# Performance work log

Measured on AMD Instinct MI355X. Metric: run time of the kernel, lower is better.

Reference implementation:

```python
import jax, jax.numpy as jnp
from jax import lax
import numpy as np

# correlation hyperparams (from init_kwargs)
MAX_D = 32      # maxDisplacement
PAD = 1         # zero padding
K = 3           # patch (kernel) size
STRIDE_K = 1    # stride over output pixels
STRIDE_D = 1    # stride over displacements


def setup_inputs() -> dict:
    key = jax.random.key(0)
    k0, k1 = jax.random.split(key)
    x0 = jax.random.normal(k0, (4, 64, 256, 512), dtype=jnp.float32)
    x1 = jax.random.normal(k1, (4, 64, 256, 512), dtype=jnp.float32)
    return {"x0": x0, "x1": x1}


def _corr2d(x0, x1):
    # x0, x1: [B, C, H, W] NCHW feature maps
    B, C, H, W = x0.shape
    # zero-pad spatially; x1 gets extra width padding so all displacements are in-bounds
    x0p = jnp.pad(x0, ((0, 0), (0, 0), (PAD, PAD), (PAD, PAD)))
    x1p = jnp.pad(x1, ((0, 0), (0, 0), (PAD, PAD), (PAD + MAX_D, PAD + MAX_D)))
    Wp = W + 2 * PAD
    # width offsets into x1p for displacements d = -MAX_D .. MAX_D step STRIDE_D
    offsets = jnp.arange(0, 2 * MAX_D + 1, STRIDE_D, dtype=jnp.int32)

    def step(carry, off):
        x1s = lax.dynamic_slice_in_dim(x1p, off, Wp, axis=3)   # [B,C,Hp,Wp]
        prod = jnp.sum(x0p * x1s, axis=1)                      # channel dot -> [B,Hp,Wp]
        # KxK box-sum over the patch, stride STRIDE_K -> [B,Ho,Wo]
        s = lax.reduce_window(prod, jnp.float32(0), lax.add,
                              (1, K, K), (1, STRIDE_K, STRIDE_K), 'VALID')
        return carry, s

    _, out = lax.scan(step, None, offsets)        # [nD, B, Ho, Wo]
    out = jnp.transpose(out, (1, 0, 2, 3))        # [B, nD, Ho, Wo]
    return out / jnp.asarray(K * K * C, out.dtype)


def reference(x0, x1):
    return _corr2d(x0, x1)
```

## Files before the change

kernel.cpp:

```cpp
#include <hip/hip_runtime.h>

#define WF 512
#define HF 256
#define CF 64
#define NDTOT 65
#define DP 72
#define APAD 40

static constexpr size_t CH  = (size_t)HF * WF;
static constexpr size_t WH  = (size_t)HF * WF;
static constexpr float  INV = 1.0f / 576.0f;

typedef _Float16 f16;
typedef _Float16 f16x2 __attribute__((ext_vector_type(2)));
typedef _Float16 f16x4 __attribute__((ext_vector_type(4)));
typedef _Float16 f16x8 __attribute__((ext_vector_type(8)));
typedef float    f32x4 __attribute__((ext_vector_type(4)));

__global__ __launch_bounds__(256, 2)
void corr_gram(const float* __restrict__ x0, const float* __restrict__ x1,
               f16* __restrict__ ws) {
    const int f = blockIdx.x;
    const int xcd = f & 7;
    const int strip = (f >> 3) & 3;
    const int pl = f >> 5;
    const int pair = xcd * 128 + pl;
    const int y = pair & 255;
    const int b = pair >> 8;

    const int t = threadIdx.x;
    const int l = t & 63;
    const int w = t >> 6;
    const int X0 = strip << 7;
    const int jb = X0 - 32;

    const int n  = l & 15;
    const int kq = l >> 4;

    __shared__ f16 S[12800];
    f16* SA = S;
    f16* SB = S + 5120;

    const float* x0r = x0 + (size_t)b * CF * CH + (size_t)y * WF;
    const float* x1r = x1 + (size_t)b * CF * CH + (size_t)y * WF;

    const int c4  = t & 31;
    const int chq = t >> 5;
    int bchp[3], bc4b[3], bcol[3]; bool bok[3];
#pragma unroll
    for (int u = 0; u < 3; ++u) {
        const int idx = u * 256 + t;
        bchp[u] = idx / 48;
        bc4b[u] = idx - 48 * bchp[u];
        bcol[u] = jb + 4 * bc4b[u];
        bok[u]  = (unsigned)bcol[u] < (unsigned)WF;
    }

#define LOADH(h, A4, B4) do { \
    const float* xa = x0r + (size_t)((h) * 32 + 4 * chq) * CH + (X0 + 4 * c4); \
    _Pragma("unroll") \
    for (int j = 0; j < 4; ++j) A4[j] = *(const f32x4*)(xa + (size_t)j * CH); \
    _Pragma("unroll") \
    for (int u = 0; u < 3; ++u) { \
        const float* xb = x1r + (size_t)((h) * 32 + 2 * bchp[u]) * CH + bcol[u]; \
        B4[2*u]     = bok[u] ? *(const f32x4*)xb        : (f32x4)0.f; \
        B4[2*u + 1] = bok[u] ? *(const f32x4*)(xb + CH) : (f32x4)0.f; \
    } \
} while (0)

#define CVTW(A4, B4) do { \
    _Pragma("unroll") \
    for (int j2 = 0; j2 < 4; ++j2) { \
        f16x4 v; \
        v[0] = (f16)A4[0][j2]; v[1] = (f16)A4[1][j2]; \
        v[2] = (f16)A4[2][j2]; v[3] = (f16)A4[3][j2]; \
        *(f16x4*)&SA[(4 * c4 + j2) * APAD + 4 * chq] = v; \
    } \
    _Pragma("unroll") \
    for (int u = 0; u < 3; ++u) { \
        _Pragma("unroll") \
        for (int j2 = 0; j2 < 4; ++j2) { \
            f16x2 v; \
            v[0] = (f16)B4[2*u][j2]; v[1] = (f16)B4[2*u + 1][j2]; \
            *(f16x2*)&SB[(4 * bc4b[u] + j2) * APAD + 2 * bchp[u]] = v; \
        } \
    } \
} while (0)

#define COMP() do { \
    const f16x8 a0 = *(const f16x8*)&SA[(w * 32 + n) * APAD + kq * 8]; \
    const f16x8 a1 = *(const f16x8*)&SA[(w * 32 + 16 + n) * APAD + kq * 8]; \
    _Pragma("unroll") \
    for (int jt = 0; jt < 6; ++jt) { \
        const f16x8 bf = *(const f16x8*)&SB[(w * 32 + jt * 16 + n) * APAD + kq * 8]; \
        if (jt < 5) \
            acc[jt] = __builtin_amdgcn_mfma_f32_16x16x32_f16(a0, bf, acc[jt], 0, 0, 0); \
        if (jt >= 1) \
            acc[4 + jt] = __builtin_amdgcn_mfma_f32_16x16x32_f16(a1, bf, acc[4 + jt], 0, 0, 0); \
    } \
} while (0)

    f32x4 acc[10];
#pragma unroll
    for (int i = 0; i < 10; ++i) acc[i] = (f32x4)0.0f;

    f32x4 a4[4], b4[6], a4n[4], b4n[6];

    LOADH(0, a4, b4);
    CVTW(a4, b4);
    __syncthreads();
    LOADH(1, a4n, b4n);
    COMP();
    __syncthreads();
    CVTW(a4n, b4n);
    __syncthreads();
    COMP();
    __syncthreads();

#undef COMP
#undef CVTW
#undef LOADH

    f16* eb = S + w * 2304;
#pragma unroll
    for (int xt = 0; xt < 2; ++xt) {
#pragma unroll
        for (int p = 0; p < 5; ++p) {
            const int i = xt * 5 + p;
#pragma unroll
            for (int q = 0; q < 4; ++q) {
                const int m = kq * 4 + q;
                const int xl = xt * 16 + m;
                const int d = 16 * p + n - m;
                if ((unsigned)d < (unsigned)NDTOT)
                    eb[xl * DP + d] = (f16)acc[i][q];
            }
        }
    }
#pragma unroll
    for (int i = 0; i < 4; ++i) {
        const int idx = l + 64 * i;
        if (idx < 224) {
            const int xl = idx / 7;
            eb[xl * DP + NDTOT + (idx - 7 * xl)] = (f16)0.f;
        }
    }
    uint4* dst = (uint4*)(ws + ((size_t)(b * HF + y) * WF + X0 + w * 32) * DP);
    const uint4* src = (const uint4*)eb;
#pragma unroll
    for (int i = 0; i < 5; ++i) {
        const int idx = l + 64 * i;
        if (idx < 288) dst[idx] = src[idx];
    }
}

__global__ __launch_bounds__(256)
void corr_box(const f16* __restrict__ ws, float* __restrict__ out) {
    const int xt = blockIdx.x;
    const int yt = blockIdx.y;
    const int b = blockIdx.z;
    const int t = threadIdx.x;
    const int x0b = xt * 32, y0 = yt * 8;

    __shared__ f16 S[10 * 34][DP];

    for (int u = 0; u < 10; ++u) {
        const int yy = y0 - 1 + u;
        const bool yok = (unsigned)yy < (unsigned)HF;
        const f16* src = ws + ((size_t)(b * HF + yy) * WF + (x0b - 1)) * DP;
#pragma unroll
        for (int sub = 0; sub < 2; ++sub) {
            const int idx = sub * 256 + t;
            if (idx < 306) {
                const int v = idx / 9, dg = idx - v * 9;
                const int xx = x0b - 1 + v;
                f16x8 val;
#pragma unroll
                for (int jj = 0; jj < 8; ++jj) val[jj] = (f16)0.f;
                if (yok && (unsigned)xx < (unsigned)WF)
                    val = *(const f16x8*)(src + (size_t)v * DP + dg * 8);
                *(f16x8*)&S[u * 34 + v][dg * 8] = val;
            }
        }
    }
    __syncthreads();

    const int ly = t >> 5, lx = t & 31;
    const int yg = y0 + ly, xg = x0b + lx;
    float* o0 = out + (size_t)b * NDTOT * WH + (size_t)yg * WF + xg;

#pragma unroll 1
    for (int dg = 0; dg < 9; ++dg) {
        f16x8 s;
#pragma unroll
        for (int jj = 0; jj < 8; ++jj) s[jj] = (f16)0.f;
#pragma unroll
        for (int du = 0; du < 3; ++du)
#pragma unroll
            for (int dv = 0; dv < 3; ++dv)
                s += *(const f16x8*)&S[(ly + du) * 34 + (lx + dv)][dg * 8];
#pragma unroll
        for (int jj = 0; jj < 8; ++jj) {
            const int d = dg * 8 + jj;
            if (d < NDTOT) o0[(size_t)d * WH] = (float)s[jj] * INV;
        }
    }
}

__global__ void corr_naive(const float* __restrict__ x0, const float* __restrict__ x1,
                           float* __restrict__ out) {
    const size_t total = (size_t)4 * NDTOT * WH;
    size_t idx = (size_t)blockIdx.x * blockDim.x + threadIdx.x;
    if (idx >= total) return;
    const int j = (int)(idx % WF);
    const int i = (int)((idx / WF) % HF);
    const int d = (int)((idx / WH) % NDTOT);
    const int b = (int)(idx / ((size_t)NDTOT * WH));
    const int disp = d - 32;
    float s = 0.f;
    for (int u = i - 1; u <= i + 1; ++u) {
        if (u < 0 || u >= HF) continue;
        for (int v = j - 1; v <= j + 1; ++v) {
            if (v < 0 || v >= WF) continue;
            const int v1c = v + disp;
            if (v1c < 0 || v1c >= WF) continue;
            const float* p0 = x0 + (size_t)b * CF * CH + (size_t)u * WF + v;
            const float* p1 = x1 + (size_t)b * CF * CH + (size_t)u * WF + v1c;
            for (int c = 0; c < CF; ++c)
                s += p0[(size_t)c * CH] * p1[(size_t)c * CH];
        }
    }
    out[idx] = s * INV;
}

extern "C" void kernel_launch(void* const* d_in, const int* in_sizes, int n_in,
                              void* d_out, int out_size, void* d_ws, size_t ws_size,
                              hipStream_t stream) {
    const float* x0 = (const float*)d_in[0];
    const float* x1 = (const float*)d_in[1];
    float* out = (float*)d_out;

    const size_t wsNeed = (size_t)4 * HF * WF * DP * sizeof(f16);

    if (ws_size >= wsNeed) {
        f16* ws = (f16*)d_ws;
        corr_gram<<<dim3(4096), dim3(256), 0, stream>>>(x0, x1, ws);
        corr_box<<<dim3(16, 32, 4), dim3(256), 0, stream>>>(ws, out);
    } else {
        const size_t total = (size_t)4 * NDTOT * WH;
        const int blocks = (int)((total + 255) / 256);
        corr_naive<<<dim3(blocks), dim3(256), 0, stream>>>(x0, x1, out);
    }
}
```

Before: 129.7 us.

## Widen gram strips to 256 columns per block and use nontemporal memory ops

The gram kernel now covers 256 output columns per block instead of 128, so each wave computes 64 columns and the 32-column halo of x1 is loaded once per wider strip. This cuts redundant x1 halo traffic and halves the grid, at the cost of a larger LDS footprint (about 41 KB) and twice the accumulator registers, which may lower occupancy. The block-to-XCD mapping changes, the x1 staging layout switches to 4-channel vectors with padding APAD=36, and workspace and output traffic now use nontemporal loads and stores to reduce cache pollution.

```diff
diff --git a/kernel.cpp b/kernel.cpp
--- a/kernel.cpp
+++ b/kernel.cpp
@@ -5,114 +5,128 @@
 #define CF 64
 #define NDTOT 65
 #define DP 72
-#define APAD 40
+#define APAD 36
 
 static constexpr size_t CH  = (size_t)HF * WF;
 static constexpr size_t WH  = (size_t)HF * WF;
 static constexpr float  INV = 1.0f / 576.0f;
 
 typedef _Float16 f16;
-typedef _Float16 f16x2 __attribute__((ext_vector_type(2)));
 typedef _Float16 f16x4 __attribute__((ext_vector_type(4)));
 typedef _Float16 f16x8 __attribute__((ext_vector_type(8)));
 typedef float    f32x4 __attribute__((ext_vector_type(4)));
-
-__global__ __launch_bounds__(256, 2)
+typedef unsigned int u32x4 __attribute__((ext_vector_type(4)));
+
+__global__ __launch_bounds__(256)
 void corr_gram(const float* __restrict__ x0, const float* __restrict__ x1,
                f16* __restrict__ ws) {
     const int f = blockIdx.x;
-    const int xcd = f & 7;
-    const int strip = (f >> 3) & 3;
-    const int pl = f >> 5;
-    const int pair = xcd * 128 + pl;
+    const int unit = (f & 7) * 256 + (f >> 3);
+    const int strip = unit & 1;
+    const int pair = unit >> 1;
     const int y = pair & 255;
     const int b = pair >> 8;
+    const int X0 = strip << 8;
 
     const int t = threadIdx.x;
     const int l = t & 63;
     const int w = t >> 6;
-    const int X0 = strip << 7;
-    const int jb = X0 - 32;
-
     const int n  = l & 15;
     const int kq = l >> 4;
 
-    __shared__ f16 S[12800];
+    __shared__ f16 S[20736];
     f16* SA = S;
-    f16* SB = S + 5120;
+    f16* SB = S + 9216;
 
     const float* x0r = x0 + (size_t)b * CF * CH + (size_t)y * WF;
     const float* x1r = x1 + (size_t)b * CF * CH + (size_t)y * WF;
 
-    const int c4  = t & 31;
-    const int chq = t >> 5;
-    int bchp[3], bc4b[3], bcol[3]; bool bok[3];
-#pragma unroll
-    for (int u = 0; u < 3; ++u) {
-        const int idx = u * 256 + t;
-        bchp[u] = idx / 48;
-        bc4b[u] = idx - 48 * bchp[u];
-        bcol[u] = jb + 4 * bc4b[u];
-        bok[u]  = (unsigned)bcol[u] < (unsigned)WF;
-    }
-
-#define LOADH(h, A4, B4) do { \
-    const float* xa = x0r + (size_t)((h) * 32 + 4 * chq) * CH + (X0 + 4 * c4); \
-    _Pragma("unroll") \
-    for (int j = 0; j < 4; ++j) A4[j] = *(const f32x4*)(xa + (size_t)j * CH); \
-    _Pragma("unroll") \
-    for (int u = 0; u < 3; ++u) { \
-        const float* xb = x1r + (size_t)((h) * 32 + 2 * bchp[u]) * CH + bcol[u]; \
-        B4[2*u]     = bok[u] ? *(const f32x4*)xb        : (f32x4)0.f; \
-        B4[2*u + 1] = bok[u] ? *(const f32x4*)(xb + CH) : (f32x4)0.f; \
+    const int cgA = t & 63, qbA = t >> 6;
+    int qB[3], cgB[3], colB[3]; bool vB[3], okB[3];
+#pragma unroll
+    for (int k = 0; k < 3; ++k) {
+        const int u = t + 256 * k;
+        vB[k] = (u < 640);
+        const int uu = vB[k] ? u : 0;
+        qB[k] = uu / 80;
+        cgB[k] = uu - 80 * qB[k];
+        const int col = X0 - 32 + 4 * cgB[k];
+        okB[k] = (col >= 0) && (col + 3 < WF);
+        colB[k] = okB[k] ? col : 0;
+    }
+
+    f32x4 acc[20];
+#pragma unroll
+    for (int i = 0; i < 20; ++i) acc[i] = (f32x4)0.0f;
+
+    f32x4 AR[8], BR[12], AR2[8], BR2[12];
+
+#define LOADH(h, A_, B_) do { \
+    _Pragma("unroll") \
+    for (int jq = 0; jq < 2; ++jq) { \
+        const int q = qbA + 4 * jq; \
+        _Pragma("unroll") \
+        for (int i = 0; i < 4; ++i) \
+            A_[4*jq+i] = *(const f32x4*)(x0r + (size_t)((h)*32 + 4*q + i) * CH + X0 + 4*cgA); \
+    } \
+    _Pragma("unroll") \
+    for (int k = 0; k < 3; ++k) { \
+        _Pragma("unroll") \
+        for (int i = 0; i < 4; ++i) \
+            B_[4*k+i] = (vB[k] && okB[k]) \
+                ? *(const f32x4*)(x1r + (size_t)((h)*32 + 4*qB[k] + i) * CH + colB[k]) \
+                : (f32x4)0.0f; \
     } \
 } while (0)
 
-#define CVTW(A4, B4) do { \
-    _Pragma("unroll") \
-    for (int j2 = 0; j2 < 4; ++j2) { \
-        f16x4 v; \
-        v[0] = (f16)A4[0][j2]; v[1] = (f16)A4[1][j2]; \
-        v[2] = (f16)A4[2][j2]; v[3] = (f16)A4[3][j2]; \
-        *(f16x4*)&SA[(4 * c4 + j2) * APAD + 4 * chq] = v; \
-    } \
-    _Pragma("unroll") \
-    for (int u = 0; u < 3; ++u) { \
+#define CVTW(A_, B_) do { \
+    _Pragma("unroll") \
+    for (int jq = 0; jq < 2; ++jq) { \
+        const int q = qbA + 4 * jq; \
         _Pragma("unroll") \
         for (int j2 = 0; j2 < 4; ++j2) { \
-            f16x2 v; \
-            v[0] = (f16)B4[2*u][j2]; v[1] = (f16)B4[2*u + 1][j2]; \
-            *(f16x2*)&SB[(4 * bc4b[u] + j2) * APAD + 2 * bchp[u]] = v; \
+            f16x4 v; \
+            v[0] = (f16)A_[4*jq+0][j2]; v[1] = (f16)A_[4*jq+1][j2]; \
+            v[2] = (f16)A_[4*jq+2][j2]; v[3] = (f16)A_[4*jq+3][j2]; \
+            *(f16x4*)&SA[(4*cgA + j2) * APAD + 4*q] = v; \
         } \
     } \
+    _Pragma("unroll") \
+    for (int k = 0; k < 3; ++k) { \
+        if (vB[k]) { \
+            _Pragma("unroll") \
+            for (int j2 = 0; j2 < 4; ++j2) { \
+                f16x4 v; \
+                v[0] = (f16)B_[4*k+0][j2]; v[1] = (f16)B_[4*k+1][j2]; \
+                v[2] = (f16)B_[4*k+2][j2]; v[3] = (f16)B_[4*k+3][j2]; \
+                *(f16x4*)&SB[(4*cgB[k] + j2) * APAD + 4*qB[k]] = v; \
+            } \
+        } \
+    } \
 } while (0)
 
 #define COMP() do { \
-    const f16x8 a0 = *(const f16x8*)&SA[(w * 32 + n) * APAD + kq * 8]; \
-    const f16x8 a1 = *(const f16x8*)&SA[(w * 32 + 16 + n) * APAD + kq * 8]; \
-    _Pragma("unroll") \
-    for (int jt = 0; jt < 6; ++jt) { \
-        const f16x8 bf = *(const f16x8*)&SB[(w * 32 + jt * 16 + n) * APAD + kq * 8]; \
-        if (jt < 5) \
-            acc[jt] = __builtin_amdgcn_mfma_f32_16x16x32_f16(a0, bf, acc[jt], 0, 0, 0); \
-        if (jt >= 1) \
-            acc[4 + jt] = __builtin_amdgcn_mfma_f32_16x16x32_f16(a1, bf, acc[4 + jt], 0, 0, 0); \
+    f16x8 a0 = *(const f16x8*)&SA[(64*w +  0 + n) * APAD + kq*8]; \
+    f16x8 a1 = *(const f16x8*)&SA[(64*w + 16 + n) * APAD + kq*8]; \
+    f16x8 a2 = *(const f16x8*)&SA[(64*w + 32 + n) * APAD + kq*8]; \
+    f16x8 a3 = *(const f16x8*)&SA[(64*w + 48 + n) * APAD + kq*8]; \
+    _Pragma("unroll") \
+    for (int jt = 0; jt < 8; ++jt) { \
+        const f16x8 bf = *(const f16x8*)&SB[(64*w + 16*jt + n) * APAD + kq*8]; \
+        if (jt - 0 >= 0 && jt - 0 < 5) acc[ 0 + jt - 0] = __builtin_amdgcn_mfma_f32_16x16x32_f16(a0, bf, acc[ 0 + jt - 0], 0, 0, 0); \
+        if (jt - 1 >= 0 && jt - 1 < 5) acc[ 5 + jt - 1] = __builtin_amdgcn_mfma_f32_16x16x32_f16(a1, bf, acc[ 5 + jt - 1], 0, 0, 0); \
+        if (jt - 2 >= 0 && jt - 2 < 5) acc[10 + jt - 2] = __builtin_amdgcn_mfma_f32_16x16x32_f16(a2, bf, acc[10 + jt - 2], 0, 0, 0); \
+        if (jt - 3 >= 0 && jt - 3 < 5) acc[15 + jt - 3] = __builtin_amdgcn_mfma_f32_16x16x32_f16(a3, bf, acc[15 + jt - 3], 0, 0, 0); \
     } \
 } while (0)
 
-    f32x4 acc[10];
-#pragma unroll
-    for (int i = 0; i < 10; ++i) acc[i] = (f32x4)0.0f;
-
-    f32x4 a4[4], b4[6], a4n[4], b4n[6];
-
-    LOADH(0, a4, b4);
-    CVTW(a4, b4);
-    __syncthreads();
-    LOADH(1, a4n, b4n);
+    LOADH(0, AR, BR);
+    CVTW(AR, BR);
+    __syncthreads();
+    LOADH(1, AR2, BR2);
     COMP();
     __syncthreads();
-    CVTW(a4n, b4n);
+    CVTW(AR2, BR2);
     __syncthreads();
     COMP();
     __syncthreads();
@@ -121,37 +135,30 @@
 #undef CVTW
 #undef LOADH
 
-    f16* eb = S + w * 2304;
-#pragma unroll
-    for (int xt = 0; xt < 2; ++xt) {
+    f16* eb = S;
+#pragma unroll
+    for (int xt = 0; xt < 4; ++xt) {
 #pragma unroll
         for (int p = 0; p < 5; ++p) {
-            const int i = xt * 5 + p;
 #pragma unroll
             for (int q = 0; q < 4; ++q) {
                 const int m = kq * 4 + q;
-                const int xl = xt * 16 + m;
+                const int xl = 64 * w + 16 * xt + m;
                 const int d = 16 * p + n - m;
                 if ((unsigned)d < (unsigned)NDTOT)
-                    eb[xl * DP + d] = (f16)acc[i][q];
+                    eb[xl * DP + d] = (f16)acc[xt * 5 + p][q];
             }
         }
     }
 #pragma unroll
-    for (int i = 0; i < 4; ++i) {
-        const int idx = l + 64 * i;
-        if (idx < 224) {
-            const int xl = idx / 7;
-            eb[xl * DP + NDTOT + (idx - 7 * xl)] = (f16)0.f;
-        }
-    }
-    uint4* dst = (uint4*)(ws + ((size_t)(b * HF + y) * WF + X0 + w * 32) * DP);
-    const uint4* src = (const uint4*)eb;
-#pragma unroll
-    for (int i = 0; i < 5; ++i) {
-        const int idx = l + 64 * i;
-        if (idx < 288) dst[idx] = src[idx];
-    }
+    for (int dd = 0; dd < 7; ++dd) eb[t * DP + NDTOT + dd] = (f16)0.f;
+    __syncthreads();
+
+    u32x4* dst = (u32x4*)(ws + ((size_t)(b * HF + y) * WF + X0) * DP);
+    const u32x4* src = (const u32x4*)eb;
+#pragma unroll
+    for (int i = 0; i < 9; ++i)
+        __builtin_nontemporal_store(src[t + 256 * i], &dst[t + 256 * i]);
 }
 
 __global__ __launch_bounds__(256)
@@ -178,7 +185,7 @@
 #pragma unroll
                 for (int jj = 0; jj < 8; ++jj) val[jj] = (f16)0.f;
                 if (yok && (unsigned)xx < (unsigned)WF)
-                    val = *(const f16x8*)(src + (size_t)v * DP + dg * 8);
+                    val = __builtin_nontemporal_load((const f16x8*)(src + (size_t)v * DP + dg * 8));
                 *(f16x8*)&S[u * 34 + v][dg * 8] = val;
             }
         }
@@ -202,7 +209,8 @@
 #pragma unroll
         for (int jj = 0; jj < 8; ++jj) {
             const int d = dg * 8 + jj;
-            if (d < NDTOT) o0[(size_t)d * WH] = (float)s[jj] * INV;
+            if (d < NDTOT)
+                __builtin_nontemporal_store((float)s[jj] * INV, &o0[(size_t)d * WH]);
         }
     }
 }
@@ -244,7 +252,7 @@
 
     if (ws_size >= wsNeed) {
         f16* ws = (f16*)d_ws;
-        corr_gram<<<dim3(4096), dim3(256), 0, stream>>>(x0, x1, ws);
+        corr_gram<<<dim3(2048), dim3(256), 0, stream>>>(x0, x1, ws);
         corr_box<<<dim3(16, 32, 4), dim3(256), 0, stream>>>(ws, out);
     } else {
         const size_t total = (size_t)4 * NDTOT * WH;
```

Measured after the change: 136.9 us. 1.06x slower.
